# Optimization experiments

Hardware: AMD Instinct MI355X
Metric: run time of the kernel (lower is better)

The kernel has to match this reference:

```python
import jax, jax.numpy as jnp
import numpy as np

B, L, C, H, K, P, NB = 32, 512, 512, 512, 16, 96, 4  # enc_in == hidden_size required by MlpBlockTimesteps
EPS = 1e-5


def setup_inputs() -> dict:
    key = jax.random.key(0)
    ks = jax.random.split(key, 12)
    g = lambda i, shape, s=0.02: jax.random.normal(ks[i], shape, jnp.float32) * s
    return {
        'x': jax.random.normal(ks[0], (B, L, C), jnp.float32),
        'rev_w': jnp.ones((C,), jnp.float32), 'rev_b': jnp.zeros((C,), jnp.float32),
        'mlp_w1': g(1, (L, H)), 'mlp_b1': jnp.zeros((H,), jnp.float32),
        'mlp_w2': g(2, (H, H)), 'mlp_b2': jnp.zeros((H,), jnp.float32),
        'cluster_embeds': jax.random.normal(ks[3], (K, H), jnp.float32),
        'wq': g(4, (H, H)), 'bq': jnp.zeros((H,), jnp.float32),
        'wk': g(5, (H, H)), 'bk': jnp.zeros((H,), jnp.float32),
        'wv': g(6, (H, H)), 'bv': jnp.zeros((H,), jnp.float32),
        'ts_ln_g': jnp.ones((C,), jnp.float32), 'ts_ln_b': jnp.zeros((C,), jnp.float32),
        'ts_w': g(7, (C, C)), 'ts_b': jnp.zeros((C,), jnp.float32),
        'ch_ln_g': jnp.ones((C,), jnp.float32), 'ch_ln_b': jnp.zeros((C,), jnp.float32),
        'ch_w1': g(8, (C, H)), 'ch_b1': jnp.zeros((H,), jnp.float32),
        'ch_w2': g(9, (H, C)), 'ch_b2': jnp.zeros((C,), jnp.float32),
        'out_w': g(10, (C, H, P)), 'out_b': jnp.zeros((C, P), jnp.float32),
    }


def _ln(z, g, b):
    m = z.mean(-1, keepdims=True)
    v = jnp.mean((z - m) ** 2, axis=-1, keepdims=True)
    return (z - m) / jnp.sqrt(v + EPS) * g + b


def _gelu(z):
    return jax.nn.gelu(z, approximate=False)


def _forward(x, rev_w, rev_b, mlp_w1, mlp_b1, mlp_w2, mlp_b2, cluster_embeds,
             wq, bq, wk, bk, wv, bv, ts_ln_g, ts_ln_b, ts_w, ts_b,
             ch_ln_g, ch_ln_b, ch_w1, ch_b1, ch_w2, ch_b2, out_w, out_b):
    # RevIN norm (stats over time dim=1)
    mean = x.mean(axis=1, keepdims=True)                      # [B,1,C]
    std = jnp.sqrt(jnp.var(x, axis=1, keepdims=True) + EPS)
    xn = (x - mean) / std * rev_w + rev_b                      # [B,L,C]
    xt = xn.transpose(0, 2, 1)                                 # [B,C,L]
    # channel MLP: Linear(L->H) -> ReLU -> Linear(H->H)
    h = jnp.maximum(xt @ mlp_w1 + mlp_b1, 0.0) @ mlp_w2 + mlp_b2  # [B,C,H]
    # cosine-sim soft routing + bernoulli hard mask
    cn = cluster_embeds / jnp.maximum(jnp.linalg.norm(cluster_embeds, axis=-1, keepdims=True), 1e-12)
    hn = h / jnp.maximum(jnp.linalg.norm(h, axis=-1, keepdims=True), 1e-12)
    p = jax.nn.softmax(hn @ cn.T, axis=-1)                     # [B,C,K]
    M = jax.random.bernoulli(jax.random.key(42), p).astype(h.dtype)
    # masked exp-attention over clusters
    Q = cluster_embeds @ wq + bq                               # [K,H]
    Kk = h @ wk + bk                                           # [B,C,H]
    V = h @ wv + bv
    scores = jnp.einsum('kh,bch->bkc', Q, Kk) / jnp.sqrt(jnp.float32(H))
    am = jnp.exp(scores) * M.transpose(0, 2, 1)                # [B,K,C]
    aw = am / am.sum(-1, keepdims=True)
    Cc = jnp.einsum('bkc,bch->bkh', aw, V)                     # [B,K,H]
    ce_new = jax.lax.stop_gradient(Cc.mean(0))                 # mimics .data.copy_ (no grad into C)
    # mixer block, NB iterations with shared weights (enc_in == hidden_size)
    Hm = h
    for _ in range(NB):
        z = Hm.transpose(0, 2, 1)                              # [B,H,C]
        Hm = (z + _gelu(_ln(z, ts_ln_g, ts_ln_b) @ ts_w + ts_b)).transpose(0, 2, 1)
        z = Hm.transpose(0, 2, 1)                              # [B,H,C]
        y2 = _gelu(_ln(z, ch_ln_g, ch_ln_b) @ ch_w1 + ch_b1) @ ch_w2 + ch_b2
        Hm = (z + y2).transpose(0, 2, 1)                       # [B,C,H]
    # per-channel expert projections gated by theta (uses UPDATED cluster embeds)
    theta = jnp.einsum('bck,kh->bch', p, ce_new)               # [B,C,H]
    y = jnp.einsum('bch,chp->bcp', Hm * theta, out_w) + out_b  # [B,C,P]
    y = y.transpose(0, 2, 1)                                   # [B,P,C]
    # RevIN denorm
    y = (y - rev_b) / (rev_w + EPS * EPS)
    return y * std + mean


def reference(x, rev_w, rev_b, mlp_w1, mlp_b1, mlp_w2, mlp_b2, cluster_embeds,
              wq, bq, wk, bk, wv, bv, ts_ln_g, ts_ln_b, ts_w, ts_b,
              ch_ln_g, ch_ln_b, ch_w1, ch_b1, ch_w2, ch_b2, out_w, out_b):
    return _forward(x, rev_w, rev_b, mlp_w1, mlp_b1, mlp_w2, mlp_b2, cluster_embeds,
                    wq, bq, wk, bk, wv, bv, ts_ln_g, ts_ln_b, ts_w, ts_b,
                    ch_ln_g, ch_ln_b, ch_w1, ch_b1, ch_w2, ch_b2, out_w, out_b)
```

## Files before the change

### kernel.cpp

```cpp
#include <hip/hip_runtime.h>
#include <math.h>

#define B_  32
#define L_  512
#define C_  512
#define H_  512
#define K_  16
#define P_  96
#define NB_ 4

typedef unsigned short u16;
typedef __attribute__((ext_vector_type(8))) __bf16 bf16x8;
typedef __attribute__((ext_vector_type(4))) float f32x4;


__device__ __forceinline__ float gelu_f(float x) {
    return 0.5f * x * (1.0f + erff(x * 0.70710678118654752440f));
}

__device__ __forceinline__ u16 f2bf(float f) {
    union { float f; unsigned u; } v; v.f = f;
    unsigned r = v.u + 0x7fffu + ((v.u >> 16) & 1u);
    return (u16)(r >> 16);
}
__device__ __forceinline__ float bf2f(u16 h) {
    union { unsigned u; float f; } v; v.u = ((unsigned)h) << 16;
    return v.f;
}

__device__ __forceinline__ void block_sum2_256(float& a, float& b) {
    __shared__ float la[4], lb[4];
    #pragma unroll
    for (int off = 32; off; off >>= 1) {
        a += __shfl_down(a, off);
        b += __shfl_down(b, off);
    }
    int wid = threadIdx.x >> 6;
    if ((threadIdx.x & 63) == 0) { la[wid] = a; lb[wid] = b; }
    __syncthreads();
    a = la[0] + la[1] + la[2] + la[3];
    b = lb[0] + lb[1] + lb[2] + lb[3];
}

__device__ __forceinline__ void threefry2x32(unsigned k0, unsigned k1,
                                             unsigned& x0, unsigned& x1) {
    const unsigned ks0 = k0, ks1 = k1, ks2 = k0 ^ k1 ^ 0x1BD11BDAu;
    x0 += ks0; x1 += ks1;
#define TF_ROT(v, r) (((v) << (r)) | ((v) >> (32 - (r))))
#define TF_R(r) { x0 += x1; x1 = TF_ROT(x1, r); x1 ^= x0; }
    TF_R(13) TF_R(15) TF_R(26) TF_R(6)   x0 += ks1; x1 += ks2 + 1u;
    TF_R(17) TF_R(29) TF_R(16) TF_R(24)  x0 += ks2; x1 += ks0 + 2u;
    TF_R(13) TF_R(15) TF_R(26) TF_R(6)   x0 += ks0; x1 += ks1 + 3u;
    TF_R(17) TF_R(29) TF_R(16) TF_R(24)  x0 += ks1; x1 += ks2 + 4u;
    TF_R(13) TF_R(15) TF_R(26) TF_R(6)   x0 += ks2; x1 += ks0 + 5u;
#undef TF_R
#undef TF_ROT
}

#define GLL16(g, l) __builtin_amdgcn_global_load_lds( \
    (const __attribute__((address_space(1))) void*)(g), \
    (__attribute__((address_space(3))) void*)(l), 16, 0, 0)


__global__ __launch_bounds__(256) void revin_stats(const float* __restrict__ x,
                                                   float* __restrict__ meanB,
                                                   float* __restrict__ stdB) {
    int b = blockIdx.x;
    int c = blockIdx.y * 256 + threadIdx.x;
    const float* xp = x + (size_t)b * L_ * C_ + c;
    float s = 0.f, ss = 0.f;
    for (int l = 0; l < L_; ++l) {
        float v = xp[(size_t)l * C_];
        s += v; ss += v * v;
    }
    float m = s * (1.0f / L_);
    float var = ss * (1.0f / L_) - m * m;
    meanB[b * C_ + c] = m;
    stdB[b * C_ + c]  = sqrtf(var + 1e-5f);
}

__global__ __launch_bounds__(256) void transpose_revin(const float* __restrict__ x,
                                                       const float* __restrict__ meanB,
                                                       const float* __restrict__ stdB,
                                                       const float* __restrict__ rw,
                                                       const float* __restrict__ rb,
                                                       u16* __restrict__ xt) {
    __shared__ float tile[32][33];
    int b = blockIdx.x, l0 = blockIdx.y * 32, c0 = blockIdx.z * 32;
    int tx = threadIdx.x, ty = threadIdx.y;
    for (int i = ty; i < 32; i += 8) {
        int l = l0 + i, c = c0 + tx;
        float v = x[((size_t)b * L_ + l) * C_ + c];
        v = (v - meanB[b * C_ + c]) / stdB[b * C_ + c] * rw[c] + rb[c];
        tile[i][tx] = v;
    }
    __syncthreads();
    for (int i = ty; i < 32; i += 8) {
        int c = c0 + i, l = l0 + tx;
        xt[((size_t)b * C_ + c) * L_ + l] = f2bf(tile[tx][i]);
    }
}

__global__ __launch_bounds__(256) void transpose_b(const float* __restrict__ in,
                                                   float* __restrict__ out) {
    __shared__ float tile[32][33];
    int b = blockIdx.x, r0 = blockIdx.y * 32, c0 = blockIdx.z * 32;
    int tx = threadIdx.x, ty = threadIdx.y;
    for (int i = ty; i < 32; i += 8)
        tile[i][tx] = in[((size_t)b * 512 + r0 + i) * 512 + c0 + tx];
    __syncthreads();
    for (int i = ty; i < 32; i += 8)
        out[((size_t)b * 512 + c0 + i) * 512 + r0 + tx] = tile[tx][i];
}

struct WPtrs { const float* src[7]; u16* dst[7]; };
__global__ __launch_bounds__(256) void convert_w(WPtrs wp) {
    __shared__ float tile[32][33];
    int wi = blockIdx.z;
    const float* src = wp.src[wi];
    u16* dst = wp.dst[wi];
    int r0 = blockIdx.y * 32, c0 = blockIdx.x * 32;
    int tx = threadIdx.x, ty = threadIdx.y;
    for (int i = ty; i < 32; i += 8)
        tile[i][tx] = src[(size_t)(r0 + i) * 512 + c0 + tx];
    __syncthreads();
    for (int i = ty; i < 32; i += 8)
        dst[(size_t)(c0 + i) * 512 + r0 + tx] = f2bf(tile[tx][i]);
}

template <int EPI>
__global__ __launch_bounds__(256) void gemm_bf16(const u16* __restrict__ A,
                                                 const u16* __restrict__ Bt,
                                                 const float* __restrict__ bias,
                                                 float* __restrict__ C32,
                                                 u16* __restrict__ C16,
                                                 int M, int N, int K) {
    __shared__ u16 As[128 * 32];
    __shared__ u16 Bs[128 * 32];
    int tid = threadIdx.x;
    int m0 = blockIdx.y * 128, n0 = blockIdx.x * 128;
    int lane = tid & 63, wave = tid >> 6;
    int wm = wave >> 1, wn = wave & 1;
    int col = lane & 15, quad = lane >> 4;
    int koff = quad * 8;

    int qa0 = tid, qa1 = tid + 256;
    const u16* Ag0 = A + (size_t)(m0 + (qa0 >> 2)) * K + (qa0 & 3) * 8;
    const u16* Ag1 = A + (size_t)(m0 + (qa1 >> 2)) * K + (qa1 & 3) * 8;
    const u16* Bg0 = Bt + (size_t)(n0 + (qa0 >> 2)) * K + (qa0 & 3) * 8;
    const u16* Bg1 = Bt + (size_t)(n0 + (qa1 >> 2)) * K + (qa1 & 3) * 8;
    u16* Al0 = &As[qa0 * 8];
    u16* Al1 = &As[qa1 * 8];
    u16* Bl0 = &Bs[qa0 * 8];
    u16* Bl1 = &Bs[qa1 * 8];

    f32x4 acc[4][4];
    #pragma unroll
    for (int i = 0; i < 4; ++i)
        #pragma unroll
        for (int j = 0; j < 4; ++j)
            acc[i][j] = (f32x4){0.f, 0.f, 0.f, 0.f};

    for (int k0 = 0; k0 < K; k0 += 32) {
        GLL16(Ag0 + k0, Al0);
        GLL16(Ag1 + k0, Al1);
        GLL16(Bg0 + k0, Bl0);
        GLL16(Bg1 + k0, Bl1);
        __syncthreads();
        bf16x8 af[4], bfr[4];
        #pragma unroll
        for (int mt = 0; mt < 4; ++mt)
            af[mt] = *(const bf16x8*)&As[(wm * 64 + mt * 16 + col) * 32 + koff];
        #pragma unroll
        for (int nt = 0; nt < 4; ++nt)
            bfr[nt] = *(const bf16x8*)&Bs[(wn * 64 + nt * 16 + col) * 32 + koff];
        #pragma unroll
        for (int mt = 0; mt < 4; ++mt)
            #pragma unroll
            for (int nt = 0; nt < 4; ++nt)
                acc[mt][nt] = __builtin_amdgcn_mfma_f32_16x16x32_bf16(
                    af[mt], bfr[nt], acc[mt][nt], 0, 0, 0);
        __syncthreads();
    }

    float bb[4];
    #pragma unroll
    for (int nt = 0; nt < 4; ++nt) bb[nt] = bias[n0 + wn * 64 + nt * 16 + col];
    #pragma unroll
    for (int mt = 0; mt < 4; ++mt) {
        int mbase = m0 + wm * 64 + mt * 16 + quad * 4;
        #pragma unroll
        for (int r = 0; r < 4; ++r) {
            size_t rowoff = (size_t)(mbase + r) * N;
            #pragma unroll
            for (int nt = 0; nt < 4; ++nt) {
                int gn = n0 + wn * 64 + nt * 16 + col;
                float t = acc[mt][nt][r] + bb[nt];
                if (EPI == 1) t = fmaxf(t, 0.f);
                if (EPI == 0) {
                    C32[rowoff + gn] = t;
                } else if (EPI == 1 || EPI == 6) {
                    C16[rowoff + gn] = f2bf(t);
                } else if (EPI == 5) {
                    C32[rowoff + gn] = t;
                    C16[rowoff + gn] = f2bf(t);
                }
            }
        }
    }
}

__global__ __launch_bounds__(256) void gemm_f32(const float* __restrict__ A,
                                                const float* __restrict__ Bm,
                                                const float* __restrict__ bias,
                                                float* __restrict__ Cm,
                                                int M, int N, int K) {
    __shared__ float As[16][64];
    __shared__ float Bs[16][64];
    int tid = threadIdx.x;
    int tx = tid & 15, ty = tid >> 4;
    int m0 = blockIdx.y * 64, n0 = blockIdx.x * 64;
    float acc[4][4] = {};
    for (int k0 = 0; k0 < K; k0 += 16) {
        {
            int r = tid >> 2, cc = (tid & 3) * 4, gm = m0 + r;
            float4 v = make_float4(0.f, 0.f, 0.f, 0.f);
            if (gm < M) v = *(const float4*)(A + (size_t)gm * K + k0 + cc);
            As[cc + 0][r] = v.x; As[cc + 1][r] = v.y;
            As[cc + 2][r] = v.z; As[cc + 3][r] = v.w;
        }
        {
            int r = tid >> 4, cc = (tid & 15) * 4;
            *(float4*)&Bs[r][cc] = *(const float4*)(Bm + (size_t)(k0 + r) * N + n0 + cc);
        }
        __syncthreads();
        #pragma unroll
        for (int kk = 0; kk < 16; ++kk) {
            float4 a4 = *(const float4*)&As[kk][ty * 4];
            float4 b4 = *(const float4*)&Bs[kk][tx * 4];
            float av[4] = {a4.x, a4.y, a4.z, a4.w};
            float bv[4] = {b4.x, b4.y, b4.z, b4.w};
            #pragma unroll
            for (int i = 0; i < 4; ++i)
                #pragma unroll
                for (int j = 0; j < 4; ++j)
                    acc[i][j] += av[i] * bv[j];
        }
        __syncthreads();
    }
    int gn = n0 + tx * 4;
    float4 b4 = *(const float4*)(bias + gn);
    float bb[4] = {b4.x, b4.y, b4.z, b4.w};
    #pragma unroll
    for (int i = 0; i < 4; ++i) {
        int gm = m0 + ty * 4 + i;
        if (gm >= M) break;
        float* cp = Cm + (size_t)gm * N + gn;
        *(float4*)cp = make_float4(acc[i][0] + bb[0], acc[i][1] + bb[1],
                                   acc[i][2] + bb[2], acc[i][3] + bb[3]);
    }
}

__global__ __launch_bounds__(256) void normalize_rows16(const float* __restrict__ ce,
                                                        float* __restrict__ cn) {
    int k = blockIdx.x, tid = threadIdx.x;
    float2 v = ((const float2*)(ce + (size_t)k * 512))[tid];
    float ss = v.x * v.x + v.y * v.y, dummy = 0.f;
    block_sum2_256(ss, dummy);
    float inv = 1.0f / fmaxf(sqrtf(ss), 1e-12f);
    float2 o; o.x = v.x * inv; o.y = v.y * inv;
    ((float2*)(cn + (size_t)k * 512))[tid] = o;
}

__global__ __launch_bounds__(256) void routing_kernel(const float* __restrict__ h,
                                                      const float* __restrict__ cn,
                                                      float* __restrict__ p) {
    int tid = threadIdx.x;
    int r = tid >> 4, k = tid & 15;
    int row = blockIdx.x * 16 + r;
    const float4* hp = (const float4*)(h + (size_t)row * 512);
    const float4* ck = (const float4*)(cn + (size_t)k * 512);
    float ss = 0.f;
    #pragma unroll
    for (int j = k * 8; j < k * 8 + 8; ++j) {
        float4 v = hp[j];
        ss += v.x * v.x + v.y * v.y + v.z * v.z + v.w * v.w;
    }
    #pragma unroll
    for (int off = 8; off; off >>= 1) ss += __shfl_xor(ss, off, 16);
    float inv = 1.0f / fmaxf(sqrtf(ss), 1e-12f);
    float d = 0.f;
    for (int j = 0; j < 128; ++j) {
        float4 a = hp[j], b = ck[j];
        d += a.x * b.x + a.y * b.y + a.z * b.z + a.w * b.w;
    }
    d *= inv;
    float mx = d;
    #pragma unroll
    for (int off = 8; off; off >>= 1) mx = fmaxf(mx, __shfl_xor(mx, off, 16));
    float e = expf(d - mx);
    float s = e;
    #pragma unroll
    for (int off = 8; off; off >>= 1) s += __shfl_xor(s, off, 16);
    p[(size_t)row * 16 + k] = e / s;
}

__global__ __launch_bounds__(256) void attn_scores(const float* __restrict__ Kk,
                                                   const float* __restrict__ Q,
                                                   const float* __restrict__ pbuf,
                                                   float* __restrict__ am) {
    int tid = threadIdx.x;
    int k = tid >> 4, r = tid & 15;
    int row = blockIdx.x * 16 + r;
    int b = row >> 9, c = row & 511;
    const float4* kp = (const float4*)(Kk + (size_t)row * 512);
    const float4* qp = (const float4*)(Q + (size_t)k * 512);
    float d = 0.f;
    for (int j = 0; j < 128; ++j) {
        float4 a = kp[j], q = qp[j];
        d += a.x * q.x + a.y * q.y + a.z * q.z + a.w * q.w;
    }
    d *= 0.044194173824159216f;
    int j = row * 16 + k;
    const int HALF = (B_ * C_ * K_) / 2;
    unsigned x0 = (j < HALF) ? (unsigned)j : (unsigned)(j - HALF);
    unsigned x1 = x0 + (unsigned)HALF;
    threefry2x32(0u, 42u, x0, x1);
    unsigned bits = (j < HALF) ? x0 : x1;
    float u = __uint_as_float((bits >> 9) | 0x3f800000u) - 1.0f;
    float m = (u < pbuf[j]) ? 1.0f : 0.0f;
    am[((size_t)b * 16 + k) * 512 + c] = expf(d) * m;
}

__global__ __launch_bounds__(256) void row_recip(const float* __restrict__ am,
                                                 float* __restrict__ recip) {
    int rk = blockIdx.x, tid = threadIdx.x;
    float2 v = ((const float2*)(am + (size_t)rk * 512))[tid];
    float s = v.x + v.y, dummy = 0.f;
    block_sum2_256(s, dummy);
    if (tid == 0) recip[rk] = 1.0f / s;
}

__global__ __launch_bounds__(256) void cc_partial(const float* __restrict__ am,
                                                  const float* __restrict__ recip,
                                                  const u16* __restrict__ V16,
                                                  float* __restrict__ Ccp) {
    int b = blockIdx.x, cs = blockIdx.y;
    int c0 = cs * 64, tid = threadIdx.x;
    __shared__ float awS[16 * 64];
    for (int idx = tid; idx < 1024; idx += 256) {
        int k = idx >> 6, cj = idx & 63;
        awS[idx] = am[((size_t)b * 16 + k) * 512 + c0 + cj] * recip[b * 16 + k];
    }
    __syncthreads();
    float acc0[16] = {}, acc1[16] = {};
    for (int cj = 0; cj < 64; ++cj) {
        const u16* vp = V16 + ((size_t)(b * 512) + c0 + cj) * 512;
        unsigned pk = ((const unsigned*)vp)[tid];
        float v0 = bf2f((u16)(pk & 0xffffu));
        float v1 = bf2f((u16)(pk >> 16));
        #pragma unroll
        for (int k = 0; k < 16; ++k) {
            float a = awS[k * 64 + cj];
            acc0[k] += a * v0;
            acc1[k] += a * v1;
        }
    }
    float* out = Ccp + ((size_t)(b * 8 + cs)) * 8192;
    #pragma unroll
    for (int k = 0; k < 16; ++k) {
        float2 o; o.x = acc0[k]; o.y = acc1[k];
        ((float2*)(out + k * 512))[tid] = o;
    }
}

__global__ __launch_bounds__(256) void cc_mean(const float* __restrict__ Ccp,
                                               float* __restrict__ ce) {
    int idx = blockIdx.x * 256 + threadIdx.x;
    float s = 0.f;
    for (int sl = 0; sl < 256; ++sl) s += Ccp[(size_t)sl * 8192 + idx];
    ce[idx] = s * (1.0f / B_);
}

__global__ __launch_bounds__(512, 4) void mixer_fused2(
    float* __restrict__ z,
    const u16* __restrict__ tsw, const u16* __restrict__ chw1,
    const u16* __restrict__ chw2,
    const float* __restrict__ tslng, const float* __restrict__ tslnb,
    const float* __restrict__ tsb,
    const float* __restrict__ chlng, const float* __restrict__ chlnb,
    const float* __restrict__ chb1, const float* __restrict__ chb2) {
    __shared__ u16 A16[32 * 520];
    __shared__ float vecS[7 * 512];
    __shared__ float partS[8 * 32 * 2];
    __shared__ float statS[32 * 2];

    int tid = threadIdx.x, lane = tid & 63, w = tid >> 6;
    int col = lane & 15, quad = lane >> 4;
    int m0 = blockIdx.x * 32;
    int nb = w * 64 + col;

    {
        const float* vsrc[7] = {tslng, tslnb, tsb, chlng, chlnb, chb1, chb2};
        for (int i = tid; i < 7 * 512; i += 512) vecS[i] = vsrc[i >> 9][i & 511];
    }

    f32x4 zr[8];
    float* zbase = z + (size_t)m0 * 512;
    #pragma unroll
    for (int mt = 0; mt < 2; ++mt)
        #pragma unroll
        for (int nt = 0; nt < 4; ++nt)
            #pragma unroll
            for (int r = 0; r < 4; ++r)
                zr[mt * 4 + nt][r] =
                    zbase[(size_t)(mt * 16 + quad * 4 + r) * 512 + nb + nt * 16];

    auto stats = [&]() {
        #pragma unroll
        for (int mt = 0; mt < 2; ++mt)
            #pragma unroll
            for (int r = 0; r < 4; ++r) {
                float s = 0.f, ss = 0.f;
                #pragma unroll
                for (int nt = 0; nt < 4; ++nt) {
                    float v = zr[mt * 4 + nt][r];
                    s += v; ss += v * v;
                }
                #pragma unroll
                for (int o = 8; o; o >>= 1) {
                    s += __shfl_xor(s, o, 16);
                    ss += __shfl_xor(ss, o, 16);
                }
                if (col == 0) {
                    int m = mt * 16 + quad * 4 + r;
                    partS[(w * 32 + m) * 2 + 0] = s;
                    partS[(w * 32 + m) * 2 + 1] = ss;
                }
            }
        __syncthreads();
        if (tid < 32) {
            float s = 0.f, ss = 0.f;
            #pragma unroll
            for (int wv = 0; wv < 8; ++wv) {
                s += partS[(wv * 32 + tid) * 2];
                ss += partS[(wv * 32 + tid) * 2 + 1];
            }
            float mean = s * (1.0f / 512.0f);
            float var = ss * (1.0f / 512.0f) - mean * mean;
            statS[tid * 2] = mean;
            statS[tid * 2 + 1] = rsqrtf(var + 1e-5f);
        }
        __syncthreads();
    };

    auto writeNorm = [&](int gi, int bi) {
        #pragma unroll
        for (int nt = 0; nt < 4; ++nt) {
            int n = nb + nt * 16;
            float g = vecS[gi * 512 + n], bb = vecS[bi * 512 + n];
            #pragma unroll
            for (int mt = 0; mt < 2; ++mt)
                #pragma unroll
                for (int r = 0; r < 4; ++r) {
                    int m = mt * 16 + quad * 4 + r;
                    float v = (zr[mt * 4 + nt][r] - statS[m * 2]) *
                              statS[m * 2 + 1] * g + bb;
                    A16[m * 520 + n] = f2bf(v);
                }
        }
        __syncthreads();
    };

    f32x4 acc[8];
    auto gemm = [&](const u16* __restrict__ W) {
        #pragma unroll
        for (int i = 0; i < 8; ++i) acc[i] = (f32x4){0.f, 0.f, 0.f, 0.f};
        const u16* wb = W + (size_t)nb * 512 + quad * 8;
        #pragma unroll 4
        for (int kc = 0; kc < 16; ++kc) {
            bf16x8 b0 = *(const bf16x8*)&wb[kc * 32];
            bf16x8 b1 = *(const bf16x8*)&wb[16 * 512 + kc * 32];
            bf16x8 b2 = *(const bf16x8*)&wb[32 * 512 + kc * 32];
            bf16x8 b3 = *(const bf16x8*)&wb[48 * 512 + kc * 32];
            bf16x8 a0 = *(const bf16x8*)&A16[col * 520 + kc * 32 + quad * 8];
            bf16x8 a1 = *(const bf16x8*)&A16[(16 + col) * 520 + kc * 32 + quad * 8];
            acc[0] = __builtin_amdgcn_mfma_f32_16x16x32_bf16(a0, b0, acc[0], 0, 0, 0);
            acc[1] = __builtin_amdgcn_mfma_f32_16x16x32_bf16(a0, b1, acc[1], 0, 0, 0);
            acc[2] = __builtin_amdgcn_mfma_f32_16x16x32_bf16(a0, b2, acc[2], 0, 0, 0);
            acc[3] = __builtin_amdgcn_mfma_f32_16x16x32_bf16(a0, b3, acc[3], 0, 0, 0);
            acc[4] = __builtin_amdgcn_mfma_f32_16x16x32_bf16(a1, b0, acc[4], 0, 0, 0);
            acc[5] = __builtin_amdgcn_mfma_f32_16x16x32_bf16(a1, b1, acc[5], 0, 0, 0);
            acc[6] = __builtin_amdgcn_mfma_f32_16x16x32_bf16(a1, b2, acc[6], 0, 0, 0);
            acc[7] = __builtin_amdgcn_mfma_f32_16x16x32_bf16(a1, b3, acc[7], 0, 0, 0);
        }
    };

    for (int it = 0; it < NB_; ++it) {
        stats();
        writeNorm(0, 1);
        gemm(tsw);
        #pragma unroll
        for (int nt = 0; nt < 4; ++nt) {
            float bb = vecS[2 * 512 + nb + nt * 16];
            #pragma unroll
            for (int mt = 0; mt < 2; ++mt)
                #pragma unroll
                for (int r = 0; r < 4; ++r)
                    zr[mt * 4 + nt][r] += gelu_f(acc[mt * 4 + nt][r] + bb);
        }
        stats();
        writeNorm(3, 4);
        gemm(chw1);
        __syncthreads();
        #pragma unroll
        for (int nt = 0; nt < 4; ++nt) {
            int n = nb + nt * 16;
            float bb = vecS[5 * 512 + n];
            #pragma unroll
            for (int mt = 0; mt < 2; ++mt)
                #pragma unroll
                for (int r = 0; r < 4; ++r) {
                    int m = mt * 16 + quad * 4 + r;
                    A16[m * 520 + n] = f2bf(gelu_f(acc[mt * 4 + nt][r] + bb));
                }
        }
        __syncthreads();
        gemm(chw2);
        #pragma unroll
        for (int nt = 0; nt < 4; ++nt) {
            float bb = vecS[6 * 512 + nb + nt * 16];
            #pragma unroll
            for (int mt = 0; mt < 2; ++mt)
                #pragma unroll
                for (int r = 0; r < 4; ++r)
                    zr[mt * 4 + nt][r] += acc[mt * 4 + nt][r] + bb;
        }
        __syncthreads();
    }

    #pragma unroll
    for (int mt = 0; mt < 2; ++mt)
        #pragma unroll
        for (int nt = 0; nt < 4; ++nt)
            #pragma unroll
            for (int r = 0; r < 4; ++r)
                zbase[(size_t)(mt * 16 + quad * 4 + r) * 512 + nb + nt * 16] =
                    zr[mt * 4 + nt][r];
}

__global__ __launch_bounds__(256) void outproj_mfma(
    const float* __restrict__ Hm, const float* __restrict__ pbuf,
    const float* __restrict__ ce, const float* __restrict__ out_w,
    const float* __restrict__ out_b, const float* __restrict__ rev_w,
    const float* __restrict__ rev_b, const float* __restrict__ meanB,
    const float* __restrict__ stdB, float* __restrict__ out) {
    __shared__ float pS[32 * 16];
    __shared__ u16 A16[32 * 520];
    __shared__ u16 Bs[4][96 * 40];
    __shared__ float redS[4][32 * 96];

    int c = blockIdx.x, tid = threadIdx.x;
    int lane = tid & 63, wave = tid >> 6;
    int col = lane & 15, quad = lane >> 4;

    for (int idx = tid; idx < 512; idx += 256) {
        int b = idx >> 4, k = idx & 15;
        pS[idx] = pbuf[((size_t)(b * 512 + c)) * 16 + k];
    }
    __syncthreads();

    {
        int h0 = lane * 8;
        f32x4 th[8][2];
        #pragma unroll
        for (int b = 0; b < 8; ++b) {
            th[b][0] = (f32x4){0.f, 0.f, 0.f, 0.f};
            th[b][1] = (f32x4){0.f, 0.f, 0.f, 0.f};
        }
        for (int k = 0; k < 16; ++k) {
            f32x4 ce0 = *(const f32x4*)&ce[k * 512 + h0];
            f32x4 ce1 = *(const f32x4*)&ce[k * 512 + h0 + 4];
            #pragma unroll
            for (int b = 0; b < 8; ++b) {
                float pk = pS[(wave * 8 + b) * 16 + k];
                th[b][0] += ce0 * pk;
                th[b][1] += ce1 * pk;
            }
        }
        #pragma unroll
        for (int b = 0; b < 8; ++b) {
            int bb = wave * 8 + b;
            const f32x4* hp = (const f32x4*)&Hm[((size_t)(bb * 512 + c)) * 512 + h0];
            f32x4 g0 = hp[0] * th[b][0];
            f32x4 g1 = hp[1] * th[b][1];
            ushort4 o0, o1;
            o0.x = f2bf(g0[0]); o0.y = f2bf(g0[1]); o0.z = f2bf(g0[2]); o0.w = f2bf(g0[3]);
            o1.x = f2bf(g1[0]); o1.y = f2bf(g1[1]); o1.z = f2bf(g1[2]); o1.w = f2bf(g1[3]);
            *(ushort4*)&A16[bb * 520 + h0] = o0;
            *(ushort4*)&A16[bb * 520 + h0 + 4] = o1;
        }
    }
    __syncthreads();

    f32x4 pacc[12];
    #pragma unroll
    for (int i = 0; i < 12; ++i) pacc[i] = (f32x4){0.f, 0.f, 0.f, 0.f};
    const size_t wbase = (size_t)c * 512 * 96;
    for (int i = 0; i < 4; ++i) {
        int kc = wave * 4 + i;
        {
            const float4* wsrc = (const float4*)(out_w + wbase + (size_t)kc * 32 * 96);
            #pragma unroll
            for (int t = 0; t < 12; ++t) {
                int flat4 = lane + t * 64;
                float4 v = wsrc[flat4];
                int kk = flat4 / 24, p4 = (flat4 % 24) * 4;
                Bs[wave][(p4 + 0) * 40 + kk] = f2bf(v.x);
                Bs[wave][(p4 + 1) * 40 + kk] = f2bf(v.y);
                Bs[wave][(p4 + 2) * 40 + kk] = f2bf(v.z);
                Bs[wave][(p4 + 3) * 40 + kk] = f2bf(v.w);
            }
        }
        __syncthreads();
        #pragma unroll
        for (int mt = 0; mt < 2; ++mt) {
            bf16x8 a = *(const bf16x8*)&A16[(mt * 16 + col) * 520 + kc * 32 + quad * 8];
            #pragma unroll
            for (int nt = 0; nt < 6; ++nt) {
                bf16x8 bf = *(const bf16x8*)&Bs[wave][(nt * 16 + col) * 40 + quad * 8];
                pacc[mt * 6 + nt] = __builtin_amdgcn_mfma_f32_16x16x32_bf16(
                    a, bf, pacc[mt * 6 + nt], 0, 0, 0);
            }
        }
        __syncthreads();
    }
    #pragma unroll
    for (int mt = 0; mt < 2; ++mt)
        #pragma unroll
        for (int nt = 0; nt < 6; ++nt)
            #pragma unroll
            for (int r = 0; r < 4; ++r) {
                int b = mt * 16 + quad * 4 + r;
                int p = nt * 16 + col;
                redS[wave][b * 96 + p] = pacc[mt * 6 + nt][r];
            }
    __syncthreads();

    float inv_rw = 1.0f / (rev_w[c] + 1e-10f);
    float rb = rev_b[c];
    for (int e = tid; e < 3072; e += 256) {
        float v = redS[0][e] + redS[1][e] + redS[2][e] + redS[3][e];
        int b = e / 96, p = e - b * 96;
        v += out_b[(size_t)c * 96 + p];
        float y = (v - rb) * inv_rw * stdB[b * 512 + c] + meanB[b * 512 + c];
        out[((size_t)b * 96 + p) * 512 + c] = y;
    }
}


extern "C" void kernel_launch(void* const* d_in, const int* in_sizes, int n_in,
                              void* d_out, int out_size, void* d_ws, size_t ws_size,
                              hipStream_t stream) {
    const float* x        = (const float*)d_in[0];
    const float* rev_w    = (const float*)d_in[1];
    const float* rev_b    = (const float*)d_in[2];
    const float* mlp_w1   = (const float*)d_in[3];
    const float* mlp_b1   = (const float*)d_in[4];
    const float* mlp_w2   = (const float*)d_in[5];
    const float* mlp_b2   = (const float*)d_in[6];
    const float* clu_emb  = (const float*)d_in[7];
    const float* wq       = (const float*)d_in[8];
    const float* bq       = (const float*)d_in[9];
    const float* wk       = (const float*)d_in[10];
    const float* bk       = (const float*)d_in[11];
    const float* wv       = (const float*)d_in[12];
    const float* bv       = (const float*)d_in[13];
    const float* ts_ln_g  = (const float*)d_in[14];
    const float* ts_ln_b  = (const float*)d_in[15];
    const float* ts_w     = (const float*)d_in[16];
    const float* ts_b     = (const float*)d_in[17];
    const float* ch_ln_g  = (const float*)d_in[18];
    const float* ch_ln_b  = (const float*)d_in[19];
    const float* ch_w1    = (const float*)d_in[20];
    const float* ch_b1    = (const float*)d_in[21];
    const float* ch_w2    = (const float*)d_in[22];
    const float* ch_b2    = (const float*)d_in[23];
    const float* out_w    = (const float*)d_in[24];
    const float* out_b    = (const float*)d_in[25];

    float* f = (float*)d_ws;
    const size_t SLOT = (size_t)(B_ * C_) * H_;
    float* F0 = f;
    float* F1 = f + SLOT;
    u16*  X16 = (u16*)(f + 2 * SLOT);
    u16*  T16 = (u16*)(f + 2 * SLOT + SLOT / 2);
    float* sm = f + 3 * SLOT;
    u16* Wt[7];
    for (int i = 0; i < 7; ++i) { Wt[i] = (u16*)sm; sm += 131072; }
    float* meanB  = sm; sm += B_ * C_;
    float* stdB   = sm; sm += B_ * C_;
    float* pbuf   = sm; sm += B_ * C_ * K_;
    float* ambuf  = sm; sm += B_ * K_ * C_;
    float* recips = sm; sm += B_ * K_;
    float* cebuf  = sm; sm += K_ * H_;
    float* cnbuf  = sm; sm += K_ * H_;
    float* Qbuf   = sm; sm += K_ * H_;
    float* Ccp = F1;

    dim3 ggrid(4, 128);
    dim3 t_grid(B_, 16, 16);
    dim3 t_blk(32, 8);
    const int Mrows = B_ * C_;

    revin_stats<<<dim3(B_, 2), 256, 0, stream>>>(x, meanB, stdB);
    transpose_revin<<<t_grid, t_blk, 0, stream>>>(x, meanB, stdB, rev_w, rev_b, X16);
    WPtrs wp;
    wp.src[0] = mlp_w1; wp.src[1] = mlp_w2; wp.src[2] = wk; wp.src[3] = wv;
    wp.src[4] = ts_w;   wp.src[5] = ch_w1;  wp.src[6] = ch_w2;
    for (int i = 0; i < 7; ++i) wp.dst[i] = Wt[i];
    convert_w<<<dim3(16, 16, 7), t_blk, 0, stream>>>(wp);
    gemm_f32<<<dim3(8, 1), 256, 0, stream>>>(clu_emb, wq, bq, Qbuf, K_, H_, H_);
    gemm_bf16<1><<<ggrid, 256, 0, stream>>>(X16, Wt[0], mlp_b1, nullptr, T16,
                                            Mrows, H_, L_);
    gemm_bf16<5><<<ggrid, 256, 0, stream>>>(T16, Wt[1], mlp_b2, F0, X16,
                                            Mrows, H_, H_);
    normalize_rows16<<<K_, 256, 0, stream>>>(clu_emb, cnbuf);
    routing_kernel<<<Mrows / 16, 256, 0, stream>>>(F0, cnbuf, pbuf);
    gemm_bf16<0><<<ggrid, 256, 0, stream>>>(X16, Wt[2], bk, F1, nullptr,
                                            Mrows, H_, H_);
    gemm_bf16<6><<<ggrid, 256, 0, stream>>>(X16, Wt[3], bv, nullptr, T16,
                                            Mrows, H_, H_);
    attn_scores<<<Mrows / 16, 256, 0, stream>>>(F1, Qbuf, pbuf, ambuf);
    row_recip<<<B_ * K_, 256, 0, stream>>>(ambuf, recips);
    cc_partial<<<dim3(B_, 8), 256, 0, stream>>>(ambuf, recips, T16, Ccp);
    cc_mean<<<(K_ * H_) / 256, 256, 0, stream>>>(Ccp, cebuf);
    transpose_b<<<t_grid, t_blk, 0, stream>>>(F0, F1);
    mixer_fused2<<<Mrows / 32, 512, 0, stream>>>(F1, Wt[4], Wt[5], Wt[6],
                                                 ts_ln_g, ts_ln_b, ts_b,
                                                 ch_ln_g, ch_ln_b, ch_b1, ch_b2);
    transpose_b<<<t_grid, t_blk, 0, stream>>>(F1, F0);
    outproj_mfma<<<C_, 256, 0, stream>>>(F0, pbuf, cebuf, out_w, out_b,
                                         rev_w, rev_b, meanB, stdB,
                                         (float*)d_out);
}
```

Before: 1.001 ms.

## Restructure mixer kernel to 1024 threads with LDS-staged weight tiles

Rewrites the fused mixer kernel to launch 16 waves per 32-row block instead of 8. Each wave now owns 16 rows by 64 columns. Weight tiles are staged into shared memory with async global-to-LDS loads (GLL16) at each k-chunk and shared by all waves, replacing per-wave direct global loads. This halves accumulator registers and cuts redundant global weight traffic. The cost is two block-wide barriers per k-chunk with no double buffering, and LN and bias vectors are now read from global memory instead of shared memory.

```diff
diff --git a/kernel.cpp b/kernel.cpp
--- a/kernel.cpp
+++ b/kernel.cpp
@@ -382,7 +382,7 @@
     ce[idx] = s * (1.0f / B_);
 }
 
-__global__ __launch_bounds__(512, 4) void mixer_fused2(
+__global__ __launch_bounds__(1024, 4) void mixer_fused4(
     float* __restrict__ z,
     const u16* __restrict__ tsw, const u16* __restrict__ chw1,
     const u16* __restrict__ chw2,
@@ -390,61 +390,55 @@
     const float* __restrict__ tsb,
     const float* __restrict__ chlng, const float* __restrict__ chlnb,
     const float* __restrict__ chb1, const float* __restrict__ chb2) {
-    __shared__ u16 A16[32 * 520];
-    __shared__ float vecS[7 * 512];
-    __shared__ float partS[8 * 32 * 2];
-    __shared__ float statS[32 * 2];
+    __shared__ u16 A16s[16 * 1024];
+    __shared__ u16 Bs[512 * 32];
+    float* partS = (float*)Bs;
+    float* statS = (float*)Bs + 512;
 
     int tid = threadIdx.x, lane = tid & 63, w = tid >> 6;
     int col = lane & 15, quad = lane >> 4;
+    int wm = w & 1, wc = w >> 1;
     int m0 = blockIdx.x * 32;
-    int nb = w * 64 + col;
-
-    {
-        const float* vsrc[7] = {tslng, tslnb, tsb, chlng, chlnb, chb1, chb2};
-        for (int i = tid; i < 7 * 512; i += 512) vecS[i] = vsrc[i >> 9][i & 511];
-    }
-
-    f32x4 zr[8];
+    int nbase = wc * 64 + col;
+
+    f32x4 zr[4];
     float* zbase = z + (size_t)m0 * 512;
     #pragma unroll
-    for (int mt = 0; mt < 2; ++mt)
-        #pragma unroll
-        for (int nt = 0; nt < 4; ++nt)
-            #pragma unroll
-            for (int r = 0; r < 4; ++r)
-                zr[mt * 4 + nt][r] =
-                    zbase[(size_t)(mt * 16 + quad * 4 + r) * 512 + nb + nt * 16];
+    for (int nt = 0; nt < 4; ++nt)
+        #pragma unroll
+        for (int r = 0; r < 4; ++r)
+            zr[nt][r] = zbase[(size_t)(wm * 16 + quad * 4 + r) * 512 +
+                              nbase + nt * 16];
 
     auto stats = [&]() {
         #pragma unroll
-        for (int mt = 0; mt < 2; ++mt)
-            #pragma unroll
-            for (int r = 0; r < 4; ++r) {
-                float s = 0.f, ss = 0.f;
-                #pragma unroll
-                for (int nt = 0; nt < 4; ++nt) {
-                    float v = zr[mt * 4 + nt][r];
-                    s += v; ss += v * v;
-                }
-                #pragma unroll
-                for (int o = 8; o; o >>= 1) {
-                    s += __shfl_xor(s, o, 16);
-                    ss += __shfl_xor(ss, o, 16);
-                }
-                if (col == 0) {
-                    int m = mt * 16 + quad * 4 + r;
-                    partS[(w * 32 + m) * 2 + 0] = s;
-                    partS[(w * 32 + m) * 2 + 1] = ss;
-                }
-            }
+        for (int r = 0; r < 4; ++r) {
+            float s = 0.f, ss = 0.f;
+            #pragma unroll
+            for (int nt = 0; nt < 4; ++nt) {
+                float v = zr[nt][r];
+                s += v; ss += v * v;
+            }
+            #pragma unroll
+            for (int o = 8; o; o >>= 1) {
+                s += __shfl_xor(s, o, 16);
+                ss += __shfl_xor(ss, o, 16);
+            }
+            if (col == 0) {
+                int rl = quad * 4 + r;
+                partS[(w * 16 + rl) * 2 + 0] = s;
+                partS[(w * 16 + rl) * 2 + 1] = ss;
+            }
+        }
         __syncthreads();
         if (tid < 32) {
+            int wmr = tid >> 4, rl = tid & 15;
             float s = 0.f, ss = 0.f;
             #pragma unroll
-            for (int wv = 0; wv < 8; ++wv) {
-                s += partS[(wv * 32 + tid) * 2];
-                ss += partS[(wv * 32 + tid) * 2 + 1];
+            for (int wcv = 0; wcv < 8; ++wcv) {
+                int wv = wcv * 2 + wmr;
+                s  += partS[(wv * 16 + rl) * 2 + 0];
+                ss += partS[(wv * 16 + rl) * 2 + 1];
             }
             float mean = s * (1.0f / 512.0f);
             float var = ss * (1.0f / 512.0f) - mean * mean;
@@ -454,99 +448,90 @@
         __syncthreads();
     };
 
-    auto writeNorm = [&](int gi, int bi) {
+    auto writeNorm = [&](const float* __restrict__ g, const float* __restrict__ b) {
         #pragma unroll
         for (int nt = 0; nt < 4; ++nt) {
-            int n = nb + nt * 16;
-            float g = vecS[gi * 512 + n], bb = vecS[bi * 512 + n];
-            #pragma unroll
-            for (int mt = 0; mt < 2; ++mt)
+            int n = nbase + nt * 16;
+            float gg = g[n], bb = b[n];
+            #pragma unroll
+            for (int r = 0; r < 4; ++r) {
+                int m = wm * 16 + quad * 4 + r;
+                float v = (zr[nt][r] - statS[m * 2]) * statS[m * 2 + 1] * gg + bb;
+                A16s[(n >> 5) * 1024 + m * 32 + (n & 31)] = f2bf(v);
+            }
+        }
+        __syncthreads();
+    };
+
+    auto gemm = [&](const u16* __restrict__ W, f32x4* acc) {
+        #pragma unroll
+        for (int i = 0; i < 4; ++i) acc[i] = (f32x4){0.f, 0.f, 0.f, 0.f};
+        for (int kc = 0; kc < 16; ++kc) {
+            int f0 = tid, f1 = tid + 1024;
+            GLL16(W + (size_t)(f0 >> 2) * 512 + kc * 32 + (f0 & 3) * 8, &Bs[f0 * 8]);
+            GLL16(W + (size_t)(f1 >> 2) * 512 + kc * 32 + (f1 & 3) * 8, &Bs[f1 * 8]);
+            __syncthreads();
+            bf16x8 a = *(const bf16x8*)&A16s[kc * 1024 + (wm * 16 + col) * 32 + quad * 8];
+            #pragma unroll
+            for (int nt = 0; nt < 4; ++nt) {
+                bf16x8 bf = *(const bf16x8*)&Bs[(nbase + nt * 16) * 32 + quad * 8];
+                acc[nt] = __builtin_amdgcn_mfma_f32_16x16x32_bf16(a, bf, acc[nt], 0, 0, 0);
+            }
+            __syncthreads();
+        }
+    };
+
+    for (int it = 0; it < NB_; ++it) {
+        stats();
+        writeNorm(tslng, tslnb);
+        {
+            f32x4 acc[4];
+            gemm(tsw, acc);
+            #pragma unroll
+            for (int nt = 0; nt < 4; ++nt) {
+                float bb = tsb[nbase + nt * 16];
+                #pragma unroll
+                for (int r = 0; r < 4; ++r)
+                    zr[nt][r] += gelu_f(acc[nt][r] + bb);
+            }
+        }
+        stats();
+        writeNorm(chlng, chlnb);
+        {
+            f32x4 acc[4];
+            gemm(chw1, acc);
+            #pragma unroll
+            for (int nt = 0; nt < 4; ++nt) {
+                int n = nbase + nt * 16;
+                float bb = chb1[n];
                 #pragma unroll
                 for (int r = 0; r < 4; ++r) {
-                    int m = mt * 16 + quad * 4 + r;
-                    float v = (zr[mt * 4 + nt][r] - statS[m * 2]) *
-                              statS[m * 2 + 1] * g + bb;
-                    A16[m * 520 + n] = f2bf(v);
+                    int m = wm * 16 + quad * 4 + r;
+                    A16s[(n >> 5) * 1024 + m * 32 + (n & 31)] =
+                        f2bf(gelu_f(acc[nt][r] + bb));
                 }
-        }
-        __syncthreads();
-    };
-
-    f32x4 acc[8];
-    auto gemm = [&](const u16* __restrict__ W) {
-        #pragma unroll
-        for (int i = 0; i < 8; ++i) acc[i] = (f32x4){0.f, 0.f, 0.f, 0.f};
-        const u16* wb = W + (size_t)nb * 512 + quad * 8;
-        #pragma unroll 4
-        for (int kc = 0; kc < 16; ++kc) {
-            bf16x8 b0 = *(const bf16x8*)&wb[kc * 32];
-            bf16x8 b1 = *(const bf16x8*)&wb[16 * 512 + kc * 32];
-            bf16x8 b2 = *(const bf16x8*)&wb[32 * 512 + kc * 32];
-            bf16x8 b3 = *(const bf16x8*)&wb[48 * 512 + kc * 32];
-            bf16x8 a0 = *(const bf16x8*)&A16[col * 520 + kc * 32 + quad * 8];
-            bf16x8 a1 = *(const bf16x8*)&A16[(16 + col) * 520 + kc * 32 + quad * 8];
-            acc[0] = __builtin_amdgcn_mfma_f32_16x16x32_bf16(a0, b0, acc[0], 0, 0, 0);
-            acc[1] = __builtin_amdgcn_mfma_f32_16x16x32_bf16(a0, b1, acc[1], 0, 0, 0);
-            acc[2] = __builtin_amdgcn_mfma_f32_16x16x32_bf16(a0, b2, acc[2], 0, 0, 0);
-            acc[3] = __builtin_amdgcn_mfma_f32_16x16x32_bf16(a0, b3, acc[3], 0, 0, 0);
-            acc[4] = __builtin_amdgcn_mfma_f32_16x16x32_bf16(a1, b0, acc[4], 0, 0, 0);
-            acc[5] = __builtin_amdgcn_mfma_f32_16x16x32_bf16(a1, b1, acc[5], 0, 0, 0);
-            acc[6] = __builtin_amdgcn_mfma_f32_16x16x32_bf16(a1, b2, acc[6], 0, 0, 0);
-            acc[7] = __builtin_amdgcn_mfma_f32_16x16x32_bf16(a1, b3, acc[7], 0, 0, 0);
-        }
-    };
-
-    for (int it = 0; it < NB_; ++it) {
-        stats();
-        writeNorm(0, 1);
-        gemm(tsw);
-        #pragma unroll
-        for (int nt = 0; nt < 4; ++nt) {
-            float bb = vecS[2 * 512 + nb + nt * 16];
-            #pragma unroll
-            for (int mt = 0; mt < 2; ++mt)
+            }
+            __syncthreads();
+        }
+        {
+            f32x4 acc[4];
+            gemm(chw2, acc);
+            #pragma unroll
+            for (int nt = 0; nt < 4; ++nt) {
+                float bb = chb2[nbase + nt * 16];
                 #pragma unroll
                 for (int r = 0; r < 4; ++r)
-                    zr[mt * 4 + nt][r] += gelu_f(acc[mt * 4 + nt][r] + bb);
-        }
-        stats();
-        writeNorm(3, 4);
-        gemm(chw1);
-        __syncthreads();
-        #pragma unroll
-        for (int nt = 0; nt < 4; ++nt) {
-            int n = nb + nt * 16;
-            float bb = vecS[5 * 512 + n];
-            #pragma unroll
-            for (int mt = 0; mt < 2; ++mt)
-                #pragma unroll
-                for (int r = 0; r < 4; ++r) {
-                    int m = mt * 16 + quad * 4 + r;
-                    A16[m * 520 + n] = f2bf(gelu_f(acc[mt * 4 + nt][r] + bb));
-                }
-        }
-        __syncthreads();
-        gemm(chw2);
-        #pragma unroll
-        for (int nt = 0; nt < 4; ++nt) {
-            float bb = vecS[6 * 512 + nb + nt * 16];
-            #pragma unroll
-            for (int mt = 0; mt < 2; ++mt)
-                #pragma unroll
-                for (int r = 0; r < 4; ++r)
-                    zr[mt * 4 + nt][r] += acc[mt * 4 + nt][r] + bb;
-        }
-        __syncthreads();
-    }
-
-    #pragma unroll
-    for (int mt = 0; mt < 2; ++mt)
-        #pragma unroll
-        for (int nt = 0; nt < 4; ++nt)
-            #pragma unroll
-            for (int r = 0; r < 4; ++r)
-                zbase[(size_t)(mt * 16 + quad * 4 + r) * 512 + nb + nt * 16] =
-                    zr[mt * 4 + nt][r];
+                    zr[nt][r] += acc[nt][r] + bb;
+            }
+        }
+    }
+
+    #pragma unroll
+    for (int nt = 0; nt < 4; ++nt)
+        #pragma unroll
+        for (int r = 0; r < 4; ++r)
+            zbase[(size_t)(wm * 16 + quad * 4 + r) * 512 + nbase + nt * 16] =
+                zr[nt][r];
 }
 
 __global__ __launch_bounds__(256) void outproj_mfma(
@@ -736,9 +721,9 @@
     cc_partial<<<dim3(B_, 8), 256, 0, stream>>>(ambuf, recips, T16, Ccp);
     cc_mean<<<(K_ * H_) / 256, 256, 0, stream>>>(Ccp, cebuf);
     transpose_b<<<t_grid, t_blk, 0, stream>>>(F0, F1);
-    mixer_fused2<<<Mrows / 32, 512, 0, stream>>>(F1, Wt[4], Wt[5], Wt[6],
-                                                 ts_ln_g, ts_ln_b, ts_b,
-                                                 ch_ln_g, ch_ln_b, ch_b1, ch_b2);
+    mixer_fused4<<<Mrows / 32, 1024, 0, stream>>>(F1, Wt[4], Wt[5], Wt[6],
+                                                  ts_ln_g, ts_ln_b, ts_b,
+                                                  ch_ln_g, ch_ln_b, ch_b1, ch_b2);
     transpose_b<<<t_grid, t_blk, 0, stream>>>(F1, F0);
     outproj_mfma<<<C_, 256, 0, stream>>>(F0, pbuf, cebuf, out_w, out_b,
                                          rev_w, rev_b, meanB, stdB,
```

Measured after the change: 1.361 ms. 35.9% more time.
